# Performance work log

Measured on AMD Instinct MI355X. Metric: run time of the kernel, lower is better.

Reference implementation:

```python
import jax, jax.numpy as jnp
import numpy as np
import math

B, H, N, DH = 4, 8, 1024, 128
DPT = 4  # point feature dim (<=4 branch: squared-distance map only)

def setup_inputs() -> dict:
    key = jax.random.key(0)
    ks = jax.random.split(key, 10)
    q   = jax.random.normal(ks[0], (B, H, N, DH), jnp.float32)
    k   = jax.random.normal(ks[1], (B, H, N, DH), jnp.float32)
    v   = jax.random.normal(ks[2], (B, H, N, DH), jnp.float32)
    c   = jax.random.normal(ks[3], (B, H, N, 1), jnp.float32)
    d_q = jax.random.normal(ks[4], (B, N, DPT), jnp.float32)
    d_k = jax.random.normal(ks[5], (B, N, DPT), jnp.float32)
    # LazyLinear(1 -> nhead): per-head scalar weight + bias
    w_w = jax.random.normal(ks[6], (H,), jnp.float32) * 0.1
    b_w = jax.random.normal(ks[7], (H,), jnp.float32) * 0.1
    w_b = jax.random.normal(ks[8], (H,), jnp.float32) * 0.1
    b_b = jax.random.normal(ks[9], (H,), jnp.float32) * 0.1
    return {"q": q, "k": k, "v": v, "c": c, "d_q": d_q, "d_k": d_k,
            "w_w": w_w, "b_w": b_w, "w_b": w_b, "b_b": b_b}

def reference(q, k, v, c, d_q, d_k, w_w, b_w, w_b, b_b):
    dh = q.shape[-1]
    # pairwise squared distances on first 3 coords (torch: under no_grad)
    dq3 = d_q[:, :, :3]
    dk3 = d_k[:, :, :3]
    dist = jax.lax.stop_gradient(
        jnp.sum(dq3 ** 2, -1)[:, :, None]
        + jnp.sum(dk3 ** 2, -1)[:, None, :]
        - 2.0 * jnp.einsum('bnd,bmd->bnm', dq3, dk3))  # [B,N,M]
    db = dist[:, None, :, :]  # [B,1,N,M]
    wbc = lambda p: p[None, :, None, None]  # [1,H,1,1]
    # distmap_w = softplus(-(w*dist + b)); distmap_b = w*dist + b (identity acts)
    distmap_w = jax.nn.softplus(-(db * wbc(w_w) + wbc(b_w)))  # [B,H,N,M]
    distmap_b = db * wbc(w_b) + wbc(b_b)                      # [B,H,N,M]
    # scaled dot-product scores per head
    scores = jnp.einsum('bhnd,bhmd->bhnm', q, k) / math.sqrt(dh)
    scores = jax.nn.relu(scores * distmap_w + distmap_b)
    detr = (jnp.sum(scores, -1, keepdims=True)
            + jnp.sum(jax.nn.softplus(c), 2, keepdims=True) + 1e-9)
    scores = scores / detr
    out = jnp.einsum('bhnm,bhmd->bhnd', scores, v)
    return out, scores
```

## Files before the change

kernel.cpp:

```cpp
#include <hip/hip_runtime.h>


typedef __attribute__((ext_vector_type(8))) short short8;
typedef __attribute__((ext_vector_type(4))) float f32x4;

#define OUT_ELEMS 4194304ull
#define WS_K      0ull
#define WS_VT     8388608ull
#define WS_CS     16777216ull

__device__ __forceinline__ unsigned short f2bf(float f) {
    unsigned u = __builtin_bit_cast(unsigned, f);
    u += 0x7FFFu + ((u >> 16) & 1u);
    return (unsigned short)(u >> 16);
}
__device__ __forceinline__ float softplus(float x) {
    return fmaxf(x, 0.f) + __logf(1.f + __expf(-fabsf(x)));
}
__device__ __forceinline__ unsigned cvt_pk_bf16(float lo, float hi) {
    unsigned r;
    asm("v_cvt_pk_bf16_f32 %0, %1, %2" : "=v"(r) : "v"(lo), "v"(hi));
    return r;
}

__global__ __launch_bounds__(256) void prep_all(
    const float* __restrict__ k, const float* __restrict__ v, const float* __restrict__ c,
    unsigned short* __restrict__ wsK, unsigned short* __restrict__ wsVt, float* __restrict__ wsCs)
{
    __shared__ unsigned short sT[64 * 132];
    const int blk = blockIdx.x, tid = threadIdx.x;
    if (blk < 512) {
        int t = blk * 256 + tid;
        for (int u = t; u < 524288; u += 131072) {
            float4 a = reinterpret_cast<const float4*>(k)[u * 2];
            float4 b = reinterpret_cast<const float4*>(k)[u * 2 + 1];
            short8 o;
            o[0]=(short)f2bf(a.x); o[1]=(short)f2bf(a.y); o[2]=(short)f2bf(a.z); o[3]=(short)f2bf(a.w);
            o[4]=(short)f2bf(b.x); o[5]=(short)f2bf(b.y); o[6]=(short)f2bf(b.z); o[7]=(short)f2bf(b.w);
            reinterpret_cast<short8*>(wsK)[u] = o;
        }
    } else if (blk < 1024) {
        const int vb = blk - 512;
        const int bh = vb >> 4, m0 = (vb & 15) * 64;
        const float* src = v + ((size_t)bh * 1024 + m0) * 128;
        for (int i = tid; i < 2048; i += 256) {
            int row = i >> 5, c4 = i & 31;
            float4 t = reinterpret_cast<const float4*>(src)[i];
            unsigned long long pk = (unsigned long long)f2bf(t.x)
                                  | ((unsigned long long)f2bf(t.y) << 16)
                                  | ((unsigned long long)f2bf(t.z) << 32)
                                  | ((unsigned long long)f2bf(t.w) << 48);
            *reinterpret_cast<unsigned long long*>(&sT[row * 132 + c4 * 4]) = pk;
        }
        __syncthreads();
        for (int u = tid; u < 2048; u += 256) {
            int dh = u >> 4, ms = u & 15;
            unsigned long long pk = (unsigned long long)sT[(ms*4+0)*132 + dh]
                                  | ((unsigned long long)sT[(ms*4+1)*132 + dh] << 16)
                                  | ((unsigned long long)sT[(ms*4+2)*132 + dh] << 32)
                                  | ((unsigned long long)sT[(ms*4+3)*132 + dh] << 48);
            *reinterpret_cast<unsigned long long*>(&wsVt[((size_t)bh * 128 + dh) * 1024 + m0 + ms * 4]) = pk;
        }
    } else {
        __shared__ float red[4];
        const int bh = blk - 1024;
        float p = 0.f;
        for (int i = tid; i < 1024; i += 256) p += softplus(c[(size_t)bh * 1024 + i]);
        p += __shfl_xor(p, 32, 64); p += __shfl_xor(p, 16, 64); p += __shfl_xor(p, 8, 64);
        p += __shfl_xor(p,  4, 64); p += __shfl_xor(p,  2, 64); p += __shfl_xor(p, 1, 64);
        if ((tid & 63) == 0) red[tid >> 6] = p;
        __syncthreads();
        if (tid == 0) wsCs[bh] = red[0] + red[1] + red[2] + red[3] + 1e-9f;
    }
}

__global__ __launch_bounds__(512, 4) void sam_main(
    const float* __restrict__ q, const float* __restrict__ dqp, const float* __restrict__ dkp,
    const float* __restrict__ w_w, const float* __restrict__ b_w,
    const float* __restrict__ w_b, const float* __restrict__ b_b,
    const unsigned short* __restrict__ wsK, const unsigned short* __restrict__ wsVt,
    const float* __restrict__ wsCs, float* __restrict__ out)
{
    __shared__ __align__(16) unsigned short sK[64 * 136];
    __shared__ __align__(16) unsigned short sVt[128 * 72];
    __shared__ __align__(16) unsigned short sP[32 * 72];
    __shared__ float sdk[4 * 64];
    __shared__ float s_red[4 * 32];
    __shared__ float s_inv[32];

    const int bid  = blockIdx.x;
    const int xcd  = bid & 7;
    const int j    = bid >> 3;
    const int bh   = xcd * 4 + (j & 3);
    const int n0   = (j >> 2) * 32;
    const int b    = bh >> 3;
    const int h    = bh & 7;
    const int tid  = threadIdx.x;
    const int lane = tid & 63;
    const int wave = tid >> 6;
    const int l15  = lane & 15;
    const int quad = lane >> 4;
    const int wr   = wave >> 2;
    const int wc   = wave & 3;
    const int mq   = wc * 16 + l15;

    const float ww = w_w[h], bw = b_w[h], wb = w_b[h], bb = b_b[h];
    const float wwn = -ww, bwn = -bw;
    const float SCALE = 0.08838834764831845f;

    unsigned short* sQ = sVt;
    {
        const float* qbase = q + ((size_t)bh * 1024 + n0) * 128;
        for (int i = tid; i < 1024; i += 512) {
            int row = i >> 5, c4 = i & 31;
            float4 t = reinterpret_cast<const float4*>(qbase)[i];
            unsigned long long pk = (unsigned long long)f2bf(t.x * SCALE)
                                  | ((unsigned long long)f2bf(t.y * SCALE) << 16)
                                  | ((unsigned long long)f2bf(t.z * SCALE) << 32)
                                  | ((unsigned long long)f2bf(t.w * SCALE) << 48);
            *reinterpret_cast<unsigned long long*>(&sQ[row * 136 + c4 * 4]) = pk;
        }
    }
    float qxm[4], qym[4], qzm[4], qs[4];
    #pragma unroll
    for (int r = 0; r < 4; r++) {
        int nl = wr * 16 + quad * 4 + r;
        float4 d4 = reinterpret_cast<const float4*>(dqp)[(size_t)b * 1024 + n0 + nl];
        qxm[r] = -2.f * d4.x; qym[r] = -2.f * d4.y; qzm[r] = -2.f * d4.z;
        qs[r] = d4.x*d4.x + d4.y*d4.y + d4.z*d4.z;
    }
    const float cs = wsCs[bh];
    __syncthreads();
    short8 afr[4];
    {
        const unsigned short* aq = &sQ[(wr * 16 + l15) * 136];
        #pragma unroll
        for (int ks = 0; ks < 4; ks++)
            afr[ks] = *reinterpret_cast<const short8*>(aq + ks * 32 + quad * 8);
    }
    __syncthreads();

    float rs[4] = {0.f, 0.f, 0.f, 0.f};
    unsigned vreg[16][2];
    #pragma unroll
    for (int t = 0; t < 16; t++) {
        const int m0 = t * 64;
        #pragma unroll
        for (int i = 0; i < 2; i++) {
            int u = tid + i * 512;
            int row = u >> 4, seg = u & 15;
            short8 d = *reinterpret_cast<const short8*>(wsK + ((size_t)bh * 1024 + m0 + row) * 128 + seg * 8);
            *reinterpret_cast<short8*>(&sK[row * 136 + seg * 8]) = d;
        }
        if (tid < 64) {
            float4 d4 = reinterpret_cast<const float4*>(dkp)[(size_t)b * 1024 + m0 + tid];
            sdk[tid] = d4.x; sdk[64 + tid] = d4.y; sdk[128 + tid] = d4.z;
            sdk[192 + tid] = d4.x*d4.x + d4.y*d4.y + d4.z*d4.z;
        }
        __syncthreads();

        f32x4 cacc = {0.f, 0.f, 0.f, 0.f};
        {
            const unsigned short* bq = &sK[(wc * 16 + l15) * 136];
            #pragma unroll
            for (int ks = 0; ks < 4; ks++) {
                short8 bfr = *reinterpret_cast<const short8*>(bq + ks * 32 + quad * 8);
                cacc = __builtin_amdgcn_mfma_f32_16x16x32_bf16(afr[ks], bfr, cacc, 0, 0, 0);
            }
        }
        const float kx = sdk[mq], ky = sdk[64 + mq], kz = sdk[128 + mq], ksq = sdk[192 + mq];
        float val[4];
        #pragma unroll
        for (int r = 0; r < 4; r++) {
            float dist = qs[r] + ksq + qxm[r]*kx + qym[r]*ky + qzm[r]*kz;
            float aw = softplus(dist * wwn + bwn);
            float ab = dist * wb + bb;
            val[r] = fmaxf(cacc[r] * aw + ab, 0.f);
            rs[r] += val[r];
        }
        vreg[t][0] = cvt_pk_bf16(val[0], val[1]);
        vreg[t][1] = cvt_pk_bf16(val[2], val[3]);
        __syncthreads();
    }

    #pragma unroll
    for (int r = 0; r < 4; r++) {
        float tsum = rs[r];
        tsum += __shfl_xor(tsum, 1, 64);
        tsum += __shfl_xor(tsum, 2, 64);
        tsum += __shfl_xor(tsum, 4, 64);
        tsum += __shfl_xor(tsum, 8, 64);
        if (l15 == 0) s_red[wc * 32 + wr * 16 + quad * 4 + r] = tsum;
    }
    __syncthreads();
    if (tid < 32) s_inv[tid] = 1.f / (s_red[tid] + s_red[32 + tid] + s_red[64 + tid] + s_red[96 + tid] + cs);
    __syncthreads();
    float inv4[4];
    #pragma unroll
    for (int r = 0; r < 4; r++) inv4[r] = s_inv[wr * 16 + quad * 4 + r];

    f32x4 oacc[2];
    oacc[0] = {0.f, 0.f, 0.f, 0.f};
    oacc[1] = {0.f, 0.f, 0.f, 0.f};
    float* scb = out + OUT_ELEMS + ((size_t)bh << 20)
               + (size_t)(n0 + wr * 16 + quad * 4) * 1024 + mq;

    #pragma unroll
    for (int t = 0; t < 16; t++) {
        const int m0 = t * 64;
        #pragma unroll
        for (int i = 0; i < 2; i++) {
            int u = tid + i * 512;
            int dh = u >> 3, seg = u & 7;
            short8 d = *reinterpret_cast<const short8*>(wsVt + ((size_t)bh * 128 + dh) * 1024 + m0 + seg * 8);
            *reinterpret_cast<short8*>(&sVt[dh * 72 + seg * 8]) = d;
        }
        {
            unsigned pv0 = vreg[t][0], pv1 = vreg[t][1];
            unsigned short vb0 = (unsigned short)pv0, vb1 = (unsigned short)(pv0 >> 16);
            unsigned short vb2 = (unsigned short)pv1, vb3 = (unsigned short)(pv1 >> 16);
            unsigned short* pbase = &sP[(wr * 16 + quad * 4) * 72 + mq];
            pbase[0]   = vb0;
            pbase[72]  = vb1;
            pbase[144] = vb2;
            pbase[216] = vb3;
            scb[m0]        = __builtin_bit_cast(float, (unsigned)vb0 << 16) * inv4[0];
            scb[m0 + 1024] = __builtin_bit_cast(float, (unsigned)vb1 << 16) * inv4[1];
            scb[m0 + 2048] = __builtin_bit_cast(float, (unsigned)vb2 << 16) * inv4[2];
            scb[m0 + 3072] = __builtin_bit_cast(float, (unsigned)vb3 << 16) * inv4[3];
        }
        __syncthreads();
        #pragma unroll
        for (int ks2 = 0; ks2 < 2; ks2++) {
            short8 pfr = *reinterpret_cast<const short8*>(&sP[(wr * 16 + l15) * 72 + ks2 * 32 + quad * 8]);
            #pragma unroll
            for (int df = 0; df < 2; df++) {
                short8 vfr = *reinterpret_cast<const short8*>(&sVt[(wc * 32 + df * 16 + l15) * 72 + ks2 * 32 + quad * 8]);
                oacc[df] = __builtin_amdgcn_mfma_f32_16x16x32_bf16(pfr, vfr, oacc[df], 0, 0, 0);
            }
        }
        __syncthreads();
    }

    {
        float* obase = out + ((size_t)bh * 1024 + n0 + wr * 16 + quad * 4) * 128 + wc * 32 + l15;
        #pragma unroll
        for (int df = 0; df < 2; df++)
            #pragma unroll
            for (int r = 0; r < 4; r++)
                obase[(size_t)r * 128 + df * 16] = oacc[df][r] * inv4[r];
    }
}

extern "C" void kernel_launch(void* const* d_in, const int* in_sizes, int n_in,
                              void* d_out, int out_size, void* d_ws, size_t ws_size,
                              hipStream_t stream) {
    const float* q   = (const float*)d_in[0];
    const float* k   = (const float*)d_in[1];
    const float* v   = (const float*)d_in[2];
    const float* c   = (const float*)d_in[3];
    const float* dq  = (const float*)d_in[4];
    const float* dk  = (const float*)d_in[5];
    const float* w_w = (const float*)d_in[6];
    const float* b_w = (const float*)d_in[7];
    const float* w_b = (const float*)d_in[8];
    const float* b_b = (const float*)d_in[9];
    float* out = (float*)d_out;
    char* ws = (char*)d_ws;
    unsigned short* wsK  = (unsigned short*)(ws + WS_K);
    unsigned short* wsVt = (unsigned short*)(ws + WS_VT);
    float* wsCs   = (float*)(ws + WS_CS);

    hipLaunchKernelGGL(prep_all, dim3(1056), dim3(256), 0, stream, k, v, c, wsK, wsVt, wsCs);
    hipLaunchKernelGGL(sam_main, dim3(1024), dim3(512), 0, stream,
                       q, dq, dk, w_w, b_w, w_b, b_b, wsK, wsVt, wsCs, out);
}
```

Before: 273.4 us.

## Load K/V MFMA fragments directly from global, double-buffer swizzled score tile

The main kernel no longer stages K and V^T tiles through shared memory. Each lane loads its MFMA B-fragments straight from the bf16 workspace in global memory, and the key-point coordinates are read per lane rather than from shared memory. This removes the per-tile barriers in the first pass. The probability tile is double-buffered in a smaller XOR-swizzled shared buffer so the scores output can be written as coalesced float4 rows. Shared memory is cut, so the occupancy hint is raised to 6 blocks per CU. The cost is redundant, less coalesced global/L2 traffic for K and V, which adds load latency inside the MFMA loops.

Result: slower. 351.7 us (+28.7%).

```diff
diff --git a/kernel.cpp b/kernel.cpp
--- a/kernel.cpp
+++ b/kernel.cpp
@@ -13,6 +13,9 @@
     unsigned u = __builtin_bit_cast(unsigned, f);
     u += 0x7FFFu + ((u >> 16) & 1u);
     return (unsigned short)(u >> 16);
+}
+__device__ __forceinline__ float bf2f(unsigned short u) {
+    return __builtin_bit_cast(float, (unsigned)u << 16);
 }
 __device__ __forceinline__ float softplus(float x) {
     return fmaxf(x, 0.f) + __logf(1.f + __expf(-fabsf(x)));
@@ -74,18 +77,15 @@
     }
 }
 
-__global__ __launch_bounds__(512, 4) void sam_main(
+__global__ __launch_bounds__(512, 6) void sam_main(
     const float* __restrict__ q, const float* __restrict__ dqp, const float* __restrict__ dkp,
     const float* __restrict__ w_w, const float* __restrict__ b_w,
     const float* __restrict__ w_b, const float* __restrict__ b_b,
     const unsigned short* __restrict__ wsK, const unsigned short* __restrict__ wsVt,
     const float* __restrict__ wsCs, float* __restrict__ out)
 {
-    __shared__ __align__(16) unsigned short sK[64 * 136];
-    __shared__ __align__(16) unsigned short sVt[128 * 72];
-    __shared__ __align__(16) unsigned short sP[32 * 72];
-    __shared__ float sdk[4 * 64];
-    __shared__ float s_red[4 * 32];
+    __shared__ __align__(16) unsigned short uS[4352];
+    __shared__ float s_red[128];
     __shared__ float s_inv[32];
 
     const int bid  = blockIdx.x;
@@ -108,7 +108,6 @@
     const float wwn = -ww, bwn = -bw;
     const float SCALE = 0.08838834764831845f;
 
-    unsigned short* sQ = sVt;
     {
         const float* qbase = q + ((size_t)bh * 1024 + n0) * 128;
         for (int i = tid; i < 1024; i += 512) {
@@ -118,7 +117,7 @@
                                   | ((unsigned long long)f2bf(t.y * SCALE) << 16)
                                   | ((unsigned long long)f2bf(t.z * SCALE) << 32)
                                   | ((unsigned long long)f2bf(t.w * SCALE) << 48);
-            *reinterpret_cast<unsigned long long*>(&sQ[row * 136 + c4 * 4]) = pk;
+            *reinterpret_cast<unsigned long long*>(&uS[row * 136 + c4 * 4]) = pk;
         }
     }
     float qxm[4], qym[4], qzm[4], qs[4];
@@ -133,46 +132,32 @@
     __syncthreads();
     short8 afr[4];
     {
-        const unsigned short* aq = &sQ[(wr * 16 + l15) * 136];
+        const unsigned short* aq = &uS[(wr * 16 + l15) * 136 + quad * 8];
         #pragma unroll
         for (int ks = 0; ks < 4; ks++)
-            afr[ks] = *reinterpret_cast<const short8*>(aq + ks * 32 + quad * 8);
-    }
-    __syncthreads();
-
+            afr[ks] = *reinterpret_cast<const short8*>(aq + ks * 32);
+    }
+    __syncthreads();
+
+    const unsigned short* kb = wsK + ((size_t)bh * 1024 + wc * 16 + l15) * 128 + quad * 8;
+    const float4* dkb = reinterpret_cast<const float4*>(dkp) + (size_t)b * 1024 + mq;
     float rs[4] = {0.f, 0.f, 0.f, 0.f};
     unsigned vreg[16][2];
     #pragma unroll
     for (int t = 0; t < 16; t++) {
-        const int m0 = t * 64;
-        #pragma unroll
-        for (int i = 0; i < 2; i++) {
-            int u = tid + i * 512;
-            int row = u >> 4, seg = u & 15;
-            short8 d = *reinterpret_cast<const short8*>(wsK + ((size_t)bh * 1024 + m0 + row) * 128 + seg * 8);
-            *reinterpret_cast<short8*>(&sK[row * 136 + seg * 8]) = d;
-        }
-        if (tid < 64) {
-            float4 d4 = reinterpret_cast<const float4*>(dkp)[(size_t)b * 1024 + m0 + tid];
-            sdk[tid] = d4.x; sdk[64 + tid] = d4.y; sdk[128 + tid] = d4.z;
-            sdk[192 + tid] = d4.x*d4.x + d4.y*d4.y + d4.z*d4.z;
-        }
-        __syncthreads();
-
         f32x4 cacc = {0.f, 0.f, 0.f, 0.f};
-        {
-            const unsigned short* bq = &sK[(wc * 16 + l15) * 136];
-            #pragma unroll
-            for (int ks = 0; ks < 4; ks++) {
-                short8 bfr = *reinterpret_cast<const short8*>(bq + ks * 32 + quad * 8);
-                cacc = __builtin_amdgcn_mfma_f32_16x16x32_bf16(afr[ks], bfr, cacc, 0, 0, 0);
-            }
-        }
-        const float kx = sdk[mq], ky = sdk[64 + mq], kz = sdk[128 + mq], ksq = sdk[192 + mq];
+        const unsigned short* kp = kb + t * 8192;
+        #pragma unroll
+        for (int ks = 0; ks < 4; ks++) {
+            short8 bfr = *reinterpret_cast<const short8*>(kp + ks * 32);
+            cacc = __builtin_amdgcn_mfma_f32_16x16x32_bf16(afr[ks], bfr, cacc, 0, 0, 0);
+        }
+        float4 d4 = dkb[t * 64];
+        float ksq = d4.x*d4.x + d4.y*d4.y + d4.z*d4.z;
         float val[4];
         #pragma unroll
         for (int r = 0; r < 4; r++) {
-            float dist = qs[r] + ksq + qxm[r]*kx + qym[r]*ky + qzm[r]*kz;
+            float dist = qs[r] + ksq + qxm[r]*d4.x + qym[r]*d4.y + qzm[r]*d4.z;
             float aw = softplus(dist * wwn + bwn);
             float ab = dist * wb + bb;
             val[r] = fmaxf(cacc[r] * aw + ab, 0.f);
@@ -180,62 +165,68 @@
         }
         vreg[t][0] = cvt_pk_bf16(val[0], val[1]);
         vreg[t][1] = cvt_pk_bf16(val[2], val[3]);
-        __syncthreads();
     }
 
     #pragma unroll
     for (int r = 0; r < 4; r++) {
-        float tsum = rs[r];
-        tsum += __shfl_xor(tsum, 1, 64);
-        tsum += __shfl_xor(tsum, 2, 64);
-        tsum += __shfl_xor(tsum, 4, 64);
-        tsum += __shfl_xor(tsum, 8, 64);
-        if (l15 == 0) s_red[wc * 32 + wr * 16 + quad * 4 + r] = tsum;
-    }
+        float ts = rs[r];
+        ts += __shfl_xor(ts, 1, 64);
+        ts += __shfl_xor(ts, 2, 64);
+        ts += __shfl_xor(ts, 4, 64);
+        ts += __shfl_xor(ts, 8, 64);
+        if (l15 == 0) s_red[wc * 32 + wr * 16 + quad * 4 + r] = ts;
+    }
+    const int r0 = wr * 16 + quad * 4;
+    const int q4 = (quad & 1) * 4;
+    unsigned short* sP = uS;
+    auto sp_write = [&](int buf, unsigned pv0, unsigned pv1) {
+        unsigned short* pb = sP + buf * 2048;
+        pb[(r0+0)*64 + (mq ^ ((q4+0) << 3))] = (unsigned short)(pv0);
+        pb[(r0+1)*64 + (mq ^ ((q4+1) << 3))] = (unsigned short)(pv0 >> 16);
+        pb[(r0+2)*64 + (mq ^ ((q4+2) << 3))] = (unsigned short)(pv1);
+        pb[(r0+3)*64 + (mq ^ ((q4+3) << 3))] = (unsigned short)(pv1 >> 16);
+    };
+    sp_write(0, vreg[0][0], vreg[0][1]);
     __syncthreads();
     if (tid < 32) s_inv[tid] = 1.f / (s_red[tid] + s_red[32 + tid] + s_red[64 + tid] + s_red[96 + tid] + cs);
     __syncthreads();
+
     float inv4[4];
     #pragma unroll
-    for (int r = 0; r < 4; r++) inv4[r] = s_inv[wr * 16 + quad * 4 + r];
+    for (int r = 0; r < 4; r++) inv4[r] = s_inv[r0 + r];
 
     f32x4 oacc[2];
     oacc[0] = {0.f, 0.f, 0.f, 0.f};
     oacc[1] = {0.f, 0.f, 0.f, 0.f};
-    float* scb = out + OUT_ELEMS + ((size_t)bh << 20)
-               + (size_t)(n0 + wr * 16 + quad * 4) * 1024 + mq;
+    const unsigned short* vb = wsVt + ((size_t)bh * 128 + wc * 32 + l15) * 1024 + quad * 8;
+    const int crow = tid >> 4, cc4 = tid & 15;
+    const int cswz = (crow & 7) << 3;
+    float* scrow = out + OUT_ELEMS + ((size_t)bh << 20) + (size_t)(n0 + crow) * 1024 + cc4 * 4;
+    const float cinv = s_inv[crow];
+    const int prow = wr * 16 + l15;
+    const int pswz = (l15 & 7) << 3;
 
     #pragma unroll
     for (int t = 0; t < 16; t++) {
-        const int m0 = t * 64;
-        #pragma unroll
-        for (int i = 0; i < 2; i++) {
-            int u = tid + i * 512;
-            int dh = u >> 3, seg = u & 7;
-            short8 d = *reinterpret_cast<const short8*>(wsVt + ((size_t)bh * 128 + dh) * 1024 + m0 + seg * 8);
-            *reinterpret_cast<short8*>(&sVt[dh * 72 + seg * 8]) = d;
-        }
+        const int cur = t & 1;
+        if (t < 15) sp_write(cur ^ 1, vreg[t + 1][0], vreg[t + 1][1]);
         {
-            unsigned pv0 = vreg[t][0], pv1 = vreg[t][1];
-            unsigned short vb0 = (unsigned short)pv0, vb1 = (unsigned short)(pv0 >> 16);
-            unsigned short vb2 = (unsigned short)pv1, vb3 = (unsigned short)(pv1 >> 16);
-            unsigned short* pbase = &sP[(wr * 16 + quad * 4) * 72 + mq];
-            pbase[0]   = vb0;
-            pbase[72]  = vb1;
-            pbase[144] = vb2;
-            pbase[216] = vb3;
-            scb[m0]        = __builtin_bit_cast(float, (unsigned)vb0 << 16) * inv4[0];
-            scb[m0 + 1024] = __builtin_bit_cast(float, (unsigned)vb1 << 16) * inv4[1];
-            scb[m0 + 2048] = __builtin_bit_cast(float, (unsigned)vb2 << 16) * inv4[2];
-            scb[m0 + 3072] = __builtin_bit_cast(float, (unsigned)vb3 << 16) * inv4[3];
-        }
-        __syncthreads();
+            unsigned long long pk = *reinterpret_cast<const unsigned long long*>(
+                &sP[cur * 2048 + crow * 64 + ((cc4 * 4) ^ cswz)]);
+            float4 o;
+            o.x = bf2f((unsigned short)(pk      )) * cinv;
+            o.y = bf2f((unsigned short)(pk >> 16)) * cinv;
+            o.z = bf2f((unsigned short)(pk >> 32)) * cinv;
+            o.w = bf2f((unsigned short)(pk >> 48)) * cinv;
+            *reinterpret_cast<float4*>(scrow + t * 64) = o;
+        }
         #pragma unroll
         for (int ks2 = 0; ks2 < 2; ks2++) {
-            short8 pfr = *reinterpret_cast<const short8*>(&sP[(wr * 16 + l15) * 72 + ks2 * 32 + quad * 8]);
+            short8 pfr = *reinterpret_cast<const short8*>(
+                &sP[cur * 2048 + prow * 64 + ((ks2 * 32 + quad * 8) ^ pswz)]);
             #pragma unroll
             for (int df = 0; df < 2; df++) {
-                short8 vfr = *reinterpret_cast<const short8*>(&sVt[(wc * 32 + df * 16 + l15) * 72 + ks2 * 32 + quad * 8]);
+                short8 vfr = *reinterpret_cast<const short8*>(vb + df * 16384 + t * 64 + ks2 * 32);
                 oacc[df] = __builtin_amdgcn_mfma_f32_16x16x32_bf16(pfr, vfr, oacc[df], 0, 0, 0);
             }
         }
@@ -243,7 +234,7 @@
     }
 
     {
-        float* obase = out + ((size_t)bh * 1024 + n0 + wr * 16 + quad * 4) * 128 + wc * 32 + l15;
+        float* obase = out + ((size_t)bh * 1024 + n0 + r0) * 128 + wc * 32 + l15;
         #pragma unroll
         for (int df = 0; df < 2; df++)
             #pragma unroll
```
